# Kernel tuning notes

Measured on AMD Instinct MI355X. Metric: run time of the kernel, lower is better.

The kernel has to match this reference:

```python
import jax, jax.numpy as jnp
import numpy as np

MARGIN = 0.3
N, D, NUM_CLASSES = 512, 256, 32


def setup_inputs() -> dict:
    key = jax.random.key(0)
    k1, k2 = jax.random.split(key)
    inputs = jax.random.normal(k1, (N, D), dtype=jnp.float32)
    targets = jax.random.randint(k2, (N,), 0, NUM_CLASSES, dtype=jnp.int64)
    return {"inputs": inputs, "targets": targets}


def reference(inputs, targets):
    # Pairwise mean-L1 distance matrix: dist[i, j] = mean_d |x_i - x_j|
    dist = jnp.mean(jnp.abs(inputs[:, None, :] - inputs[None, :, :]), axis=-1)  # (n, n)
    # Positive mask: same label (diagonal included, dist 0 there -> harmless for max)
    mask = targets[:, None] == targets[None, :]  # (n, n) bool
    # Hard mining: hardest positive (max over same-class), hardest negative (min over diff-class)
    dist_ap = jnp.max(jnp.where(mask, dist, -jnp.inf), axis=1)  # (n,)
    dist_an = jnp.min(jnp.where(mask, jnp.inf, dist), axis=1)   # (n,)
    # MarginRankingLoss with y = 1: mean(max(0, -(dist_an - dist_ap) + margin))
    loss = jnp.mean(jnp.maximum(dist_ap - dist_an + MARGIN, 0.0))
    return loss
```

## Files before the change

kernel.cpp:

```cpp
#include <hip/hip_runtime.h>
#include <math.h>

#define N 512
#define D 256
#define LOSS_MARGIN 0.3f
#define TI 16
#define TJ 32
#define STRIDE 260

__global__ __launch_bounds__(256) void triplet_tile_kernel(
    const float* __restrict__ X,
    const int*  __restrict__ tgt,
    float* __restrict__ wap,
    float* __restrict__ wan)
{
    const int it = blockIdx.x;
    const int jt = blockIdx.y;
    const int t  = threadIdx.x;

    __shared__ float tile[(TI + TJ) * STRIDE];
    __shared__ float sap[4][16], san[4][16];

    const int i0 = it * TI, j0 = jt * TJ;

    #pragma unroll
    for (int k = 0; k < 12; ++k) {
        const int f = t + 256 * k;
        const int r = f >> 6;
        const int c = (f & 63) << 2;
        const int grow = (r < TI) ? (i0 + r) : (j0 + (r - TI));
        const float4 v = *(const float4*)(X + grow * D + c);
        *(float4*)(&tile[r * STRIDE + c]) = v;
    }
    __syncthreads();

    const int il = t & 15;
    const int jl = t >> 4;
    const int ci  = tgt[i0 + il];
    const int cj0 = tgt[j0 + jl];
    const int cj1 = tgt[j0 + jl + 16];

    const float4* xi  = (const float4*)&tile[il * STRIDE];
    const float4* xj0 = (const float4*)&tile[(TI + jl) * STRIDE];
    const float4* xj1 = (const float4*)&tile[(TI + jl + 16) * STRIDE];

    float4 acc0 = {0.f, 0.f, 0.f, 0.f};
    float4 acc1 = {0.f, 0.f, 0.f, 0.f};

    #pragma unroll 8
    for (int d = 0; d < D / 4; ++d) {
        const float4 a = xi[d];
        const float4 b = xj0[d];
        const float4 c = xj1[d];
        acc0.x += fabsf(a.x - b.x);  acc0.y += fabsf(a.y - b.y);
        acc0.z += fabsf(a.z - b.z);  acc0.w += fabsf(a.w - b.w);
        acc1.x += fabsf(a.x - c.x);  acc1.y += fabsf(a.y - c.y);
        acc1.z += fabsf(a.z - c.z);  acc1.w += fabsf(a.w - c.w);
    }
    const float d0 = (acc0.x + acc0.y + acc0.z + acc0.w) * (1.0f / (float)D);
    const float d1 = (acc1.x + acc1.y + acc1.z + acc1.w) * (1.0f / (float)D);

    float ap = fmaxf(cj0 == ci ? d0 : -INFINITY, cj1 == ci ? d1 : -INFINITY);
    float an = fminf(cj0 == ci ?  INFINITY : d0, cj1 == ci ?  INFINITY : d1);

    ap = fmaxf(ap, __shfl_xor(ap, 16, 64));
    an = fminf(an, __shfl_xor(an, 16, 64));
    ap = fmaxf(ap, __shfl_xor(ap, 32, 64));
    an = fminf(an, __shfl_xor(an, 32, 64));

    const int w = t >> 6, wl = t & 63;
    if (wl < 16) { sap[w][wl] = ap; san[w][wl] = an; }
    __syncthreads();

    if (t < 16) {
        const float A  = fmaxf(fmaxf(sap[0][t], sap[1][t]), fmaxf(sap[2][t], sap[3][t]));
        const float Nn = fminf(fminf(san[0][t], san[1][t]), fminf(san[2][t], san[3][t]));
        wap[jt * N + i0 + t] = A;
        wan[jt * N + i0 + t] = Nn;
    }
}

__global__ __launch_bounds__(512) void triplet_final_kernel(
    const float* __restrict__ wap, const float* __restrict__ wan,
    float* __restrict__ out)
{
    const int t = threadIdx.x;
    float ap = -INFINITY, an = INFINITY;
    #pragma unroll
    for (int jt = 0; jt < 16; ++jt) {
        ap = fmaxf(ap, wap[jt * N + t]);
        an = fminf(an, wan[jt * N + t]);
    }
    float v = fmaxf(ap - an + LOSS_MARGIN, 0.0f);
    #pragma unroll
    for (int off = 32; off >= 1; off >>= 1) v += __shfl_down(v, off, 64);
    __shared__ float s[8];
    if ((t & 63) == 0) s[t >> 6] = v;
    __syncthreads();
    if (t == 0) {
        float tot = 0.f;
        #pragma unroll
        for (int w = 0; w < 8; ++w) tot += s[w];
        out[0] = tot * (1.0f / (float)N);
    }
}

extern "C" void kernel_launch(void* const* d_in, const int* in_sizes, int n_in,
                              void* d_out, int out_size, void* d_ws, size_t ws_size,
                              hipStream_t stream) {
    const float* X   = (const float*)d_in[0];
    const int*   tgt = (const int*)d_in[1];
    float* out = (float*)d_out;
    float* wap = (float*)d_ws;
    float* wan = wap + 16 * N;

    dim3 grid(32, 16);
    triplet_tile_kernel<<<grid, 256, 0, stream>>>(X, tgt, wap, wan);
    triplet_final_kernel<<<1, 512, 0, stream>>>(wap, wan, out);
}
```

Before: 63.11 us.

## Use 32x32 tiles with 2x2 register blocking and read j rows from global

```diff
diff --git a/kernel.cpp b/kernel.cpp
--- a/kernel.cpp
+++ b/kernel.cpp
@@ -4,8 +4,6 @@
 #define N 512
 #define D 256
 #define LOSS_MARGIN 0.3f
-#define TI 16
-#define TJ 32
 #define STRIDE 260
 
 __global__ __launch_bounds__(256) void triplet_tile_kernel(
@@ -14,65 +12,67 @@
     float* __restrict__ wap,
     float* __restrict__ wan)
 {
-    const int it = blockIdx.x;
-    const int jt = blockIdx.y;
-    const int t  = threadIdx.x;
+    const int it = blockIdx.x, jt = blockIdx.y, t = threadIdx.x;
+    const int i0 = it * 32, j0 = jt * 32;
 
-    __shared__ float tile[(TI + TJ) * STRIDE];
-    __shared__ float sap[4][16], san[4][16];
-
-    const int i0 = it * TI, j0 = jt * TJ;
+    __shared__ float xi[32 * STRIDE];
+    __shared__ float sap[4][32], san[4][32];
 
     #pragma unroll
-    for (int k = 0; k < 12; ++k) {
+    for (int k = 0; k < 8; ++k) {
         const int f = t + 256 * k;
-        const int r = f >> 6;
-        const int c = (f & 63) << 2;
-        const int grow = (r < TI) ? (i0 + r) : (j0 + (r - TI));
-        const float4 v = *(const float4*)(X + grow * D + c);
-        *(float4*)(&tile[r * STRIDE + c]) = v;
+        const int r = f >> 6, c = (f & 63) << 2;
+        *(float4*)&xi[r * STRIDE + c] = *(const float4*)(X + (i0 + r) * D + c);
     }
     __syncthreads();
 
-    const int il = t & 15;
-    const int jl = t >> 4;
-    const int ci  = tgt[i0 + il];
-    const int cj0 = tgt[j0 + jl];
-    const int cj1 = tgt[j0 + jl + 16];
+    const int il = t & 15, jl = t >> 4;
+    const int ci0 = tgt[i0 + il], ci1 = tgt[i0 + il + 16];
+    const int cj0 = tgt[j0 + jl], cj1 = tgt[j0 + jl + 16];
 
-    const float4* xi  = (const float4*)&tile[il * STRIDE];
-    const float4* xj0 = (const float4*)&tile[(TI + jl) * STRIDE];
-    const float4* xj1 = (const float4*)&tile[(TI + jl + 16) * STRIDE];
+    const float4* a0p = (const float4*)&xi[il * STRIDE];
+    const float4* a1p = (const float4*)&xi[(il + 16) * STRIDE];
+    const float4* b0p = (const float4*)(X + (j0 + jl) * D);
+    const float4* b1p = (const float4*)(X + (j0 + jl + 16) * D);
 
-    float4 acc0 = {0.f, 0.f, 0.f, 0.f};
-    float4 acc1 = {0.f, 0.f, 0.f, 0.f};
+    float4 s00 = {0,0,0,0}, s01 = {0,0,0,0}, s10 = {0,0,0,0}, s11 = {0,0,0,0};
+    #pragma unroll 4
+    for (int d = 0; d < D / 4; ++d) {
+        const float4 a0 = a0p[d], a1 = a1p[d];
+        const float4 b0 = b0p[d], b1 = b1p[d];
+        s00.x += fabsf(a0.x-b0.x); s00.y += fabsf(a0.y-b0.y);
+        s00.z += fabsf(a0.z-b0.z); s00.w += fabsf(a0.w-b0.w);
+        s01.x += fabsf(a0.x-b1.x); s01.y += fabsf(a0.y-b1.y);
+        s01.z += fabsf(a0.z-b1.z); s01.w += fabsf(a0.w-b1.w);
+        s10.x += fabsf(a1.x-b0.x); s10.y += fabsf(a1.y-b0.y);
+        s10.z += fabsf(a1.z-b0.z); s10.w += fabsf(a1.w-b0.w);
+        s11.x += fabsf(a1.x-b1.x); s11.y += fabsf(a1.y-b1.y);
+        s11.z += fabsf(a1.z-b1.z); s11.w += fabsf(a1.w-b1.w);
+    }
+    const float inv = 1.0f / (float)D;
+    const float d00 = (s00.x+s00.y+s00.z+s00.w) * inv;
+    const float d01 = (s01.x+s01.y+s01.z+s01.w) * inv;
+    const float d10 = (s10.x+s10.y+s10.z+s10.w) * inv;
+    const float d11 = (s11.x+s11.y+s11.z+s11.w) * inv;
 
-    #pragma unroll 8
-    for (int d = 0; d < D / 4; ++d) {
-        const float4 a = xi[d];
-        const float4 b = xj0[d];
-        const float4 c = xj1[d];
-        acc0.x += fabsf(a.x - b.x);  acc0.y += fabsf(a.y - b.y);
-        acc0.z += fabsf(a.z - b.z);  acc0.w += fabsf(a.w - b.w);
-        acc1.x += fabsf(a.x - c.x);  acc1.y += fabsf(a.y - c.y);
-        acc1.z += fabsf(a.z - c.z);  acc1.w += fabsf(a.w - c.w);
-    }
-    const float d0 = (acc0.x + acc0.y + acc0.z + acc0.w) * (1.0f / (float)D);
-    const float d1 = (acc1.x + acc1.y + acc1.z + acc1.w) * (1.0f / (float)D);
+    float ap0 = fmaxf(cj0==ci0 ? d00 : -INFINITY, cj1==ci0 ? d01 : -INFINITY);
+    float an0 = fminf(cj0==ci0 ?  INFINITY : d00, cj1==ci0 ?  INFINITY : d01);
+    float ap1 = fmaxf(cj0==ci1 ? d10 : -INFINITY, cj1==ci1 ? d11 : -INFINITY);
+    float an1 = fminf(cj0==ci1 ?  INFINITY : d10, cj1==ci1 ?  INFINITY : d11);
 
-    float ap = fmaxf(cj0 == ci ? d0 : -INFINITY, cj1 == ci ? d1 : -INFINITY);
-    float an = fminf(cj0 == ci ?  INFINITY : d0, cj1 == ci ?  INFINITY : d1);
-
-    ap = fmaxf(ap, __shfl_xor(ap, 16, 64));
-    an = fminf(an, __shfl_xor(an, 16, 64));
-    ap = fmaxf(ap, __shfl_xor(ap, 32, 64));
-    an = fminf(an, __shfl_xor(an, 32, 64));
+    ap0 = fmaxf(ap0, __shfl_xor(ap0, 16, 64)); an0 = fminf(an0, __shfl_xor(an0, 16, 64));
+    ap1 = fmaxf(ap1, __shfl_xor(ap1, 16, 64)); an1 = fminf(an1, __shfl_xor(an1, 16, 64));
+    ap0 = fmaxf(ap0, __shfl_xor(ap0, 32, 64)); an0 = fminf(an0, __shfl_xor(an0, 32, 64));
+    ap1 = fmaxf(ap1, __shfl_xor(ap1, 32, 64)); an1 = fminf(an1, __shfl_xor(an1, 32, 64));
 
     const int w = t >> 6, wl = t & 63;
-    if (wl < 16) { sap[w][wl] = ap; san[w][wl] = an; }
+    if (wl < 16) {
+        sap[w][wl]      = ap0;  san[w][wl]      = an0;
+        sap[w][wl + 16] = ap1;  san[w][wl + 16] = an1;
+    }
     __syncthreads();
 
-    if (t < 16) {
+    if (t < 32) {
         const float A  = fmaxf(fmaxf(sap[0][t], sap[1][t]), fmaxf(sap[2][t], sap[3][t]));
         const float Nn = fminf(fminf(san[0][t], san[1][t]), fminf(san[2][t], san[3][t]));
         wap[jt * N + i0 + t] = A;
@@ -114,7 +114,7 @@
     float* wap = (float*)d_ws;
     float* wan = wap + 16 * N;
 
-    dim3 grid(32, 16);
+    dim3 grid(16, 16);
     triplet_tile_kernel<<<grid, 256, 0, stream>>>(X, tgt, wap, wan);
-    triplet_final_kernel<<<1, 512, 0, stream>>>(wap, wan, out);
+    triplet_final_kernel<<<1, N, 0, stream>>>(wap, wan, out);
 }
```

New measurement: 64.47 us. 1.02x slower.
